# Kernel tuning notes

Measured on AMD Instinct MI355X. Metric: run time of the kernel, lower is better.

The kernel has to match this reference:

```python
import jax, jax.numpy as jnp
import numpy as np

D_MODEL = 1024
D_STATE = 64
BATCH = 4
SEQ_L = 4096
LN_EPS = 1e-5


def setup_inputs() -> dict:
    key = jax.random.key(0)
    ks = jax.random.split(key, 8)
    u = jax.random.normal(ks[0], (BATCH, SEQ_L, D_MODEL), jnp.float32)
    # Parameters mirroring StateSpaceLayer._initialize_parameters
    A_log = jax.random.uniform(ks[1], (D_STATE,), jnp.float32, -2.0, -0.1)
    xav = float(np.sqrt(6.0 / (D_STATE + D_MODEL)))
    B = jax.random.uniform(ks[2], (D_STATE, D_MODEL), jnp.float32, -xav, xav) * 0.1
    C = jax.random.uniform(ks[3], (D_MODEL, D_STATE), jnp.float32, -xav, xav) * 0.1
    D = jnp.zeros((D_MODEL,), jnp.float32)
    delta = jax.random.uniform(ks[4], (D_MODEL,), jnp.float32, 0.001, 0.1)
    gamma = jnp.ones((D_MODEL,), jnp.float32)
    beta = jnp.zeros((D_MODEL,), jnp.float32)
    freq_align = jax.random.normal(ks[5], (D_MODEL,), jnp.float32)
    reward = jax.random.normal(ks[6], (D_MODEL,), jnp.float32)
    return dict(u=u, A_log=A_log, B=B, C=C, D=D, delta=delta,
                gamma=gamma, beta=beta, freq_align=freq_align, reward=reward)


def reference(u, A_log, B, C, D, delta, gamma, beta, freq_align, reward):
    b, L, d = u.shape
    A = -jnp.exp(A_log)                                   # [N]
    # --- convolution kernel: K[k] = C @ (A_bar[0])^k, A_bar[0] = exp(delta[0]*A) ---
    k_idx = jnp.arange(L, dtype=u.dtype)                  # [L]
    powers = jnp.exp(k_idx[:, None] * (delta[0] * A)[None, :])  # [L, N]
    K = jnp.einsum('ln,dn->ld', powers, C)                # [L, D]
    # --- FFT-based causal (circular, zero-padded) convolution ---
    fft_size = 1 << int(np.ceil(np.log2(2 * L)))
    u_fft = jnp.fft.fft(u, n=fft_size, axis=1)            # [B, F, D] complex
    K_fft = jnp.fft.fft(K, n=fft_size, axis=0)            # [F, D] complex
    y = jnp.fft.ifft(u_fft * K_fft[None], axis=1).real[:, :L, :]
    # --- D skip connection ---
    y = y + u * D
    # --- FFT-based learning signals: scale spectrum, add real 'reward' to every bin ---
    y_fft = jnp.fft.fft(y, axis=1)
    y = jnp.fft.ifft(y_fft * freq_align + reward, axis=1).real
    # --- LayerNorm (eval-mode dropout = identity) ---
    mean = y.mean(-1, keepdims=True)
    var = y.var(-1, keepdims=True)
    y = (y - mean) / jnp.sqrt(var + LN_EPS) * gamma + beta
    # --- final state update with mean timescale ---
    delta_mean = delta.mean()
    A_bar_s = jnp.exp(delta_mean * A)                     # [N]
    A_safe = A + 1e-8 * jnp.sign(A)
    B_bar = ((A_bar_s - 1.0) / A_safe)[:, None] * B       # [N, D]
    state = jnp.zeros((b, A.shape[0]), u.dtype)
    final_state = A_bar_s * state + jnp.einsum('nd,bd->bn', B_bar, u[:, -1, :])
    return (y, final_state)
```

## Files before the change

### kernel.cpp

```cpp
#include <hip/hip_runtime.h>
#include <math.h>

#define BATCH  4
#define SEQL   4096
#define DMODEL 1024
#define NSTATE 64
#define LN_EPS 1e-5f
#define TB     16

typedef unsigned short u16;
typedef unsigned int   u32;
typedef float f32x2 __attribute__((ext_vector_type(2)));

__device__ __forceinline__ f32x2 fma2(f32x2 a, f32x2 b, f32x2 c) {
#if __has_builtin(__builtin_elementwise_fma)
    return __builtin_elementwise_fma(a, b, c);
#else
    f32x2 d; d.x = fmaf(a.x, b.x, c.x); d.y = fmaf(a.y, b.y, c.y); return d;
#endif
}

__device__ __forceinline__ u16 f2bf(float x) {
    u32 b = __float_as_uint(x);
    b += 0x7FFF + ((b >> 16) & 1);
    return (u16)(b >> 16);
}
__device__ __forceinline__ float bf2f(u16 h) {
    return __uint_as_float(((u32)h) << 16);
}

__global__ __launch_bounds__(256) void k_local_state(const float* __restrict__ u,
                                                     const float* __restrict__ A_log,
                                                     const float* __restrict__ delta,
                                                     const float* __restrict__ Bm,
                                                     u16* __restrict__ f,
                                                     float* __restrict__ st,
                                                     int NCH, int TCH, int nb) {
    if (blockIdx.x >= nb) {
        const int sb = blockIdx.x - nb;
        const int n = sb & 63;
        const int b = sb >> 6;
        const int tid = threadIdx.x;
        const float* ul = u + ((size_t)b * SEQL + (SEQL - 1)) * DMODEL;
        const float* Bn = Bm + (size_t)n * DMODEL;
        float dot = 0.f, dsum = 0.f;
        for (int dd = tid; dd < DMODEL; dd += 256) {
            dot = fmaf(Bn[dd], ul[dd], dot);
            dsum += delta[dd];
        }
#pragma unroll
        for (int off = 32; off > 0; off >>= 1) {
            dot  += __shfl_down(dot,  off, 64);
            dsum += __shfl_down(dsum, off, 64);
        }
        __shared__ float red[8];
        const int wave = tid >> 6, lane = tid & 63;
        if (lane == 0) { red[wave] = dot; red[4 + wave] = dsum; }
        __syncthreads();
        if (tid == 0) {
            dot  = red[0] + red[1] + red[2] + red[3];
            dsum = red[4] + red[5] + red[6] + red[7];
            const float dmean = dsum * (1.f / DMODEL);
            const float A = -expf(A_log[n]);
            const float Abar = expf(dmean * A);
            const float Asafe = A + (A >= 0.f ? 1e-8f : -1e-8f);
            st[sb] = ((Abar - 1.f) / Asafe) * dot;
        }
        return;
    }
    __shared__ float r_lds[NSTATE];
    const int tid = threadIdx.x;
    const int w = tid >> 6, l = tid & 63;
    const int b   = blockIdx.x / (16 * NCH);
    const int rem = blockIdx.x % (16 * NCH);
    const int dt  = rem / NCH;
    const int j   = rem % NCH;
    const int n0  = w << 4;
    const int d   = (dt << 6) | l;

    if (tid < NSTATE) r_lds[tid] = expf(delta[0] * -expf(A_log[tid]));
    __syncthreads();

    f32x2 r2[8], s2[8];
#pragma unroll
    for (int p = 0; p < 8; ++p) {
        r2[p] = *(const f32x2*)&r_lds[n0 + 2 * p];
        s2[p] = (f32x2)(0.f, 0.f);
    }

    const float* ub = u + ((size_t)b * SEQL + (size_t)j * TCH) * DMODEL + d;
    for (int tb = 0; tb < TCH / TB; ++tb) {
        float ur[TB];
#pragma unroll
        for (int t = 0; t < TB; ++t)
            ur[t] = ub[(size_t)(tb * TB + t) * DMODEL];
#pragma unroll
        for (int q = 0; q < 4; ++q) {
            f32x2 sa = s2[2*q], sb2 = s2[2*q+1];
            const f32x2 ra = r2[2*q], rb = r2[2*q+1];
#pragma unroll
            for (int t = 0; t < TB; ++t) {
                f32x2 u2; u2.x = ur[t]; u2.y = ur[t];
                sa  = fma2(ra, sa,  u2);
                sb2 = fma2(rb, sb2, u2);
            }
            s2[2*q] = sa; s2[2*q+1] = sb2;
        }
    }
    u16* fb = f + (((size_t)b * NCH + j) * NSTATE + n0) * DMODEL + d;
#pragma unroll
    for (int p = 0; p < 8; ++p) {
        fb[(size_t)(2*p)     * DMODEL] = f2bf(s2[p].x);
        fb[(size_t)(2*p + 1) * DMODEL] = f2bf(s2[p].y);
    }
}

template <bool ZBF16>
__global__ __launch_bounds__(256) void k_replay(const float* __restrict__ u,
                                                const float* __restrict__ A_log,
                                                const float* __restrict__ C,
                                                const float* __restrict__ Dvec,
                                                const float* __restrict__ delta,
                                                const u16* __restrict__ f,
                                                const float* __restrict__ fal,
                                                const float* __restrict__ rw,
                                                void* __restrict__ zout,
                                                int NCH, int TCH) {
    __shared__ float r_lds[NSTATE];
    __shared__ float rT_lds[NSTATE];
    __shared__ float part[2][4][TB][64];
    const int tid = threadIdx.x;
    const int w = tid >> 6, l = tid & 63;
    const int b   = blockIdx.x / (16 * NCH);
    const int rem = blockIdx.x % (16 * NCH);
    const int dt  = rem / NCH;
    const int j   = rem % NCH;
    const int n0  = w << 4;
    const int d   = (dt << 6) | l;

    if (tid < NSTATE) {
        const float A = -expf(A_log[tid]);
        const float d0v = delta[0];
        r_lds[tid]  = expf(d0v * A);
        rT_lds[tid] = expf((float)TCH * d0v * A);
    }
    __syncthreads();

    const float fad = fal[d];
    f32x2 r2[8], c2[8], s2[8];
#pragma unroll
    for (int p = 0; p < 8; ++p) {
        r2[p] = *(const f32x2*)&r_lds[n0 + 2 * p];
        s2[p] = (f32x2)(0.f, 0.f);
    }
#pragma unroll
    for (int p = 0; p < 8; ++p) {
        c2[p].x = fad * C[(size_t)d * NSTATE + n0 + 2*p];
        c2[p].y = fad * C[(size_t)d * NSTATE + n0 + 2*p + 1];
    }

    {
        f32x2 rT2[8];
#pragma unroll
        for (int p = 0; p < 8; ++p)
            rT2[p] = *(const f32x2*)&rT_lds[n0 + 2 * p];
        const u16* fbase = f + ((size_t)b * NCH * NSTATE + n0) * DMODEL + d;
        const size_t kstride = (size_t)NSTATE * DMODEL;
#pragma unroll 1
        for (int k = 0; k < j; ++k) {
            const u16* fk = fbase + (size_t)k * kstride;
#pragma unroll
            for (int p = 0; p < 8; ++p) {
                f32x2 fv;
                fv.x = bf2f(fk[(size_t)(2*p)     * DMODEL]);
                fv.y = bf2f(fk[(size_t)(2*p + 1) * DMODEL]);
                s2[p] = fma2(rT2[p], s2[p], fv);
            }
        }
    }

    const float Ddf = Dvec[d] * fad;
    const float rwd = rw[d];
    const float* ub = u + ((size_t)b * SEQL + (size_t)j * TCH) * DMODEL + d;
    const size_t zoff = ((size_t)b * SEQL + (size_t)j * TCH) * DMODEL + d;
    u16*   zb16 = (u16*)zout + zoff;
    float* zb32 = (float*)zout + zoff;

    for (int tb = 0; tb < TCH / TB; ++tb) {
        const int pb = tb & 1;
        float ur[TB];
        f32x2 zr2[TB];
#pragma unroll
        for (int t = 0; t < TB; ++t) {
            ur[t] = ub[(size_t)(tb * TB + t) * DMODEL];
            zr2[t] = (f32x2)(0.f, 0.f);
        }
#pragma unroll
        for (int q = 0; q < 4; ++q) {
            f32x2 sa = s2[2*q], sb2 = s2[2*q+1];
            const f32x2 ra = r2[2*q], rb = r2[2*q+1];
            const f32x2 ca = c2[2*q], cb = c2[2*q+1];
#pragma unroll
            for (int t = 0; t < TB; ++t) {
                f32x2 u2; u2.x = ur[t]; u2.y = ur[t];
                sa  = fma2(ra, sa,  u2);
                sb2 = fma2(rb, sb2, u2);
                zr2[t] = fma2(ca, sa,  zr2[t]);
                zr2[t] = fma2(cb, sb2, zr2[t]);
            }
            s2[2*q] = sa; s2[2*q+1] = sb2;
        }
#pragma unroll
        for (int t = 0; t < TB; ++t) {
            float v = zr2[t].x + zr2[t].y;
            if (w == 0) v = fmaf(Ddf, ur[t], v);
            part[pb][w][t][l] = v;
        }
        __syncthreads();
#pragma unroll
        for (int k = 0; k < 4; ++k) {
            const int t = (w << 2) | k;
            float v = (part[pb][0][t][l] + part[pb][1][t][l]) +
                      (part[pb][2][t][l] + part[pb][3][t][l]);
            if (j == 0 && tb == 0 && t == 0) v += rwd;
            if (ZBF16) zb16[(size_t)(tb * TB + t) * DMODEL] = f2bf(v);
            else       zb32[(size_t)(tb * TB + t) * DMODEL] = v;
        }
    }
}

template <bool ZBF16>
__global__ __launch_bounds__(256) void k_ln(const void* __restrict__ zin,
                                            float* __restrict__ y,
                                            const float* __restrict__ gamma,
                                            const float* __restrict__ beta) {
    const int tid = threadIdx.x;
    float4 v;
    if (ZBF16) {
        const ushort4 h = ((const ushort4*)((const u16*)zin + (size_t)blockIdx.x * DMODEL))[tid];
        v.x = bf2f(h.x); v.y = bf2f(h.y); v.z = bf2f(h.z); v.w = bf2f(h.w);
    } else {
        v = ((const float4*)((const float*)zin + (size_t)blockIdx.x * DMODEL))[tid];
    }
    float sum = v.x + v.y + v.z + v.w;
    float sq  = v.x*v.x + v.y*v.y + v.z*v.z + v.w*v.w;
#pragma unroll
    for (int off = 32; off > 0; off >>= 1) {
        sum += __shfl_down(sum, off, 64);
        sq  += __shfl_down(sq,  off, 64);
    }
    __shared__ float red[8];
    const int wave = tid >> 6, lane = tid & 63;
    if (lane == 0) { red[wave] = sum; red[4 + wave] = sq; }
    __syncthreads();
    sum = red[0] + red[1] + red[2] + red[3];
    sq  = red[4] + red[5] + red[6] + red[7];
    const float mean = sum * (1.f / DMODEL);
    const float var  = sq * (1.f / DMODEL) - mean * mean;
    const float inv  = 1.f / sqrtf(var + LN_EPS);
    const float4 g  = ((const float4*)gamma)[tid];
    const float4 bb = ((const float4*)beta)[tid];
    float4 o;
    o.x = (v.x - mean) * inv * g.x + bb.x;
    o.y = (v.y - mean) * inv * g.y + bb.y;
    o.z = (v.z - mean) * inv * g.z + bb.z;
    o.w = (v.w - mean) * inv * g.w + bb.w;
    ((float4*)(y + (size_t)blockIdx.x * DMODEL))[tid] = o;
}

extern "C" void kernel_launch(void* const* d_in, const int* in_sizes, int n_in,
                              void* d_out, int out_size, void* d_ws, size_t ws_size,
                              hipStream_t stream) {
    const float* u     = (const float*)d_in[0];
    const float* A_log = (const float*)d_in[1];
    const float* B     = (const float*)d_in[2];
    const float* C     = (const float*)d_in[3];
    const float* Dv    = (const float*)d_in[4];
    const float* delta = (const float*)d_in[5];
    const float* gamma = (const float*)d_in[6];
    const float* beta  = (const float*)d_in[7];
    const float* fal   = (const float*)d_in[8];
    const float* rw    = (const float*)d_in[9];

    float* y  = (float*)d_out;
    float* st = y + (size_t)BATCH * SEQL * DMODEL;
    u16* f    = (u16*)d_ws;

    int NCH = 16;
    while (NCH > 4 && (size_t)BATCH * NCH * NSTATE * DMODEL * sizeof(u16) > ws_size)
        NCH >>= 1;
    const int TCH = SEQL / NCH;
    const int nb = BATCH * 16 * NCH;

    const size_t f_bytes = (size_t)BATCH * NCH * NSTATE * DMODEL * sizeof(u16);
    const size_t z_bytes = (size_t)BATCH * SEQL * DMODEL * sizeof(u16);
    const bool zbf16 = (f_bytes + z_bytes) <= ws_size;
    void* zbuf = zbf16 ? (void*)((char*)d_ws + f_bytes) : (void*)y;

    hipLaunchKernelGGL(k_local_state, dim3(nb + BATCH * NSTATE), dim3(256), 0, stream,
                       u, A_log, delta, B, f, st, NCH, TCH, nb);
    if (zbf16) {
        hipLaunchKernelGGL((k_replay<true>), dim3(nb), dim3(256), 0, stream,
                           u, A_log, C, Dv, delta, f, fal, rw, zbuf, NCH, TCH);
        hipLaunchKernelGGL((k_ln<true>), dim3(BATCH * SEQL), dim3(256), 0, stream,
                           zbuf, y, gamma, beta);
    } else {
        hipLaunchKernelGGL((k_replay<false>), dim3(nb), dim3(256), 0, stream,
                           u, A_log, C, Dv, delta, f, fal, rw, zbuf, NCH, TCH);
        hipLaunchKernelGGL((k_ln<false>), dim3(BATCH * SEQL), dim3(256), 0, stream,
                           zbuf, y, gamma, beta);
    }
}
```

Before: 120.2 us.

## Restructure chunked scan: local scan first, carry pass, then fused correction+LayerNorm

Replaces the local-state pass plus replay pass with a single chunk-local scan that writes the partial output z and each chunk's end state. A small kernel then scans the chunk carries across chunks and stores C-weighted carries. A fused kernel adds the carry's decayed contribution to z and applies LayerNorm, with eight rows per block. This removes the second full read of u and the per-chunk O(j) carry replay, at the cost of a 64-state correction GEMV per row in the LayerNorm kernel and an extra launch. NCH is now fixed at 16 instead of adapting to workspace size.

```diff
diff --git a/kernel.cpp b/kernel.cpp
--- a/kernel.cpp
+++ b/kernel.cpp
@@ -6,7 +6,10 @@
 #define DMODEL 1024
 #define NSTATE 64
 #define LN_EPS 1e-5f
+#define NCH    16
+#define TCH    256
 #define TB     16
+#define TSUB   8
 
 typedef unsigned short u16;
 typedef unsigned int   u32;
@@ -28,14 +31,23 @@
 __device__ __forceinline__ float bf2f(u16 h) {
     return __uint_as_float(((u32)h) << 16);
 }
-
-__global__ __launch_bounds__(256) void k_local_state(const float* __restrict__ u,
-                                                     const float* __restrict__ A_log,
-                                                     const float* __restrict__ delta,
-                                                     const float* __restrict__ Bm,
-                                                     u16* __restrict__ f,
-                                                     float* __restrict__ st,
-                                                     int NCH, int TCH, int nb) {
+__device__ __forceinline__ f32x2 unpack2bf(u32 p) {
+    f32x2 v; v.x = bf2f((u16)p); v.y = bf2f((u16)(p >> 16)); return v;
+}
+
+template <bool ZBF16>
+__global__ __launch_bounds__(256) void k_scan(const float* __restrict__ u,
+                                              const float* __restrict__ A_log,
+                                              const float* __restrict__ C,
+                                              const float* __restrict__ Dvec,
+                                              const float* __restrict__ delta,
+                                              const float* __restrict__ fal,
+                                              const float* __restrict__ rw,
+                                              const float* __restrict__ Bm,
+                                              u16* __restrict__ f,
+                                              void* __restrict__ zout,
+                                              float* __restrict__ st,
+                                              int nb) {
     if (blockIdx.x >= nb) {
         const int sb = blockIdx.x - nb;
         const int n = sb & 63;
@@ -69,65 +81,6 @@
         return;
     }
     __shared__ float r_lds[NSTATE];
-    const int tid = threadIdx.x;
-    const int w = tid >> 6, l = tid & 63;
-    const int b   = blockIdx.x / (16 * NCH);
-    const int rem = blockIdx.x % (16 * NCH);
-    const int dt  = rem / NCH;
-    const int j   = rem % NCH;
-    const int n0  = w << 4;
-    const int d   = (dt << 6) | l;
-
-    if (tid < NSTATE) r_lds[tid] = expf(delta[0] * -expf(A_log[tid]));
-    __syncthreads();
-
-    f32x2 r2[8], s2[8];
-#pragma unroll
-    for (int p = 0; p < 8; ++p) {
-        r2[p] = *(const f32x2*)&r_lds[n0 + 2 * p];
-        s2[p] = (f32x2)(0.f, 0.f);
-    }
-
-    const float* ub = u + ((size_t)b * SEQL + (size_t)j * TCH) * DMODEL + d;
-    for (int tb = 0; tb < TCH / TB; ++tb) {
-        float ur[TB];
-#pragma unroll
-        for (int t = 0; t < TB; ++t)
-            ur[t] = ub[(size_t)(tb * TB + t) * DMODEL];
-#pragma unroll
-        for (int q = 0; q < 4; ++q) {
-            f32x2 sa = s2[2*q], sb2 = s2[2*q+1];
-            const f32x2 ra = r2[2*q], rb = r2[2*q+1];
-#pragma unroll
-            for (int t = 0; t < TB; ++t) {
-                f32x2 u2; u2.x = ur[t]; u2.y = ur[t];
-                sa  = fma2(ra, sa,  u2);
-                sb2 = fma2(rb, sb2, u2);
-            }
-            s2[2*q] = sa; s2[2*q+1] = sb2;
-        }
-    }
-    u16* fb = f + (((size_t)b * NCH + j) * NSTATE + n0) * DMODEL + d;
-#pragma unroll
-    for (int p = 0; p < 8; ++p) {
-        fb[(size_t)(2*p)     * DMODEL] = f2bf(s2[p].x);
-        fb[(size_t)(2*p + 1) * DMODEL] = f2bf(s2[p].y);
-    }
-}
-
-template <bool ZBF16>
-__global__ __launch_bounds__(256) void k_replay(const float* __restrict__ u,
-                                                const float* __restrict__ A_log,
-                                                const float* __restrict__ C,
-                                                const float* __restrict__ Dvec,
-                                                const float* __restrict__ delta,
-                                                const u16* __restrict__ f,
-                                                const float* __restrict__ fal,
-                                                const float* __restrict__ rw,
-                                                void* __restrict__ zout,
-                                                int NCH, int TCH) {
-    __shared__ float r_lds[NSTATE];
-    __shared__ float rT_lds[NSTATE];
     __shared__ float part[2][4][TB][64];
     const int tid = threadIdx.x;
     const int w = tid >> 6, l = tid & 63;
@@ -138,12 +91,7 @@
     const int n0  = w << 4;
     const int d   = (dt << 6) | l;
 
-    if (tid < NSTATE) {
-        const float A = -expf(A_log[tid]);
-        const float d0v = delta[0];
-        r_lds[tid]  = expf(d0v * A);
-        rT_lds[tid] = expf((float)TCH * d0v * A);
-    }
+    if (tid < NSTATE) r_lds[tid] = expf(delta[0] * -expf(A_log[tid]));
     __syncthreads();
 
     const float fad = fal[d];
@@ -157,26 +105,6 @@
     for (int p = 0; p < 8; ++p) {
         c2[p].x = fad * C[(size_t)d * NSTATE + n0 + 2*p];
         c2[p].y = fad * C[(size_t)d * NSTATE + n0 + 2*p + 1];
-    }
-
-    {
-        f32x2 rT2[8];
-#pragma unroll
-        for (int p = 0; p < 8; ++p)
-            rT2[p] = *(const f32x2*)&rT_lds[n0 + 2 * p];
-        const u16* fbase = f + ((size_t)b * NCH * NSTATE + n0) * DMODEL + d;
-        const size_t kstride = (size_t)NSTATE * DMODEL;
-#pragma unroll 1
-        for (int k = 0; k < j; ++k) {
-            const u16* fk = fbase + (size_t)k * kstride;
-#pragma unroll
-            for (int p = 0; p < 8; ++p) {
-                f32x2 fv;
-                fv.x = bf2f(fk[(size_t)(2*p)     * DMODEL]);
-                fv.y = bf2f(fk[(size_t)(2*p + 1) * DMODEL]);
-                s2[p] = fma2(rT2[p], s2[p], fv);
-            }
-        }
     }
 
     const float Ddf = Dvec[d] * fad;
@@ -227,45 +155,142 @@
             else       zb32[(size_t)(tb * TB + t) * DMODEL] = v;
         }
     }
+    u16* fb = f + (((size_t)b * NCH + j) * NSTATE + n0) * DMODEL + d;
+#pragma unroll
+    for (int p = 0; p < 8; ++p) {
+        fb[(size_t)(2*p)     * DMODEL] = f2bf(s2[p].x);
+        fb[(size_t)(2*p + 1) * DMODEL] = f2bf(s2[p].y);
+    }
+}
+
+__global__ __launch_bounds__(256) void k_pass2w(const float* __restrict__ A_log,
+                                                const float* __restrict__ delta,
+                                                const float* __restrict__ C,
+                                                const float* __restrict__ fal,
+                                                u16* __restrict__ f) {
+    const int tid = blockIdx.x * 256 + threadIdx.x;
+    const int d = tid & (DMODEL - 1);
+    const int n = (tid >> 10) & (NSTATE - 1);
+    const int b = tid >> 16;
+    const float A  = -expf(A_log[n]);
+    const float rT = expf((float)TCH * delta[0] * A);
+    const float fc = fal[d] * C[(size_t)d * NSTATE + n];
+    float I = 0.f;
+    u16* p = f + ((size_t)b * NCH * NSTATE + n) * DMODEL + d;
+    const size_t stride = (size_t)NSTATE * DMODEL;
+    for (int j = 0; j < NCH; ++j) {
+        float tmp = bf2f(p[(size_t)j * stride]);
+        p[(size_t)j * stride] = f2bf(fc * I);
+        I = fmaf(rT, I, tmp);
+    }
 }
 
 template <bool ZBF16>
-__global__ __launch_bounds__(256) void k_ln(const void* __restrict__ zin,
-                                            float* __restrict__ y,
-                                            const float* __restrict__ gamma,
-                                            const float* __restrict__ beta) {
+__global__ __launch_bounds__(256) void k_corr_ln(const void* __restrict__ zin,
+                                                 const u16* __restrict__ W,
+                                                 const float* __restrict__ A_log,
+                                                 const float* __restrict__ delta,
+                                                 const float* __restrict__ gamma,
+                                                 const float* __restrict__ beta,
+                                                 float* __restrict__ y) {
+    const int lb  = (blockIdx.x & 7) * 256 + (blockIdx.x >> 3);
+    const int b   = lb >> 9;
+    const int row = lb & 511;
+    const int tbase = row * TSUB;
+    const int j     = tbase >> 8;
+    const int tloc0 = tbase & (TCH - 1);
+
+    __shared__ float r_lds[NSTATE];
+    __shared__ float pst_lds[NSTATE];
+    __shared__ float red[4 * TSUB * 2];
+
     const int tid = threadIdx.x;
-    float4 v;
-    if (ZBF16) {
-        const ushort4 h = ((const ushort4*)((const u16*)zin + (size_t)blockIdx.x * DMODEL))[tid];
-        v.x = bf2f(h.x); v.y = bf2f(h.y); v.z = bf2f(h.z); v.w = bf2f(h.w);
-    } else {
-        v = ((const float4*)((const float*)zin + (size_t)blockIdx.x * DMODEL))[tid];
-    }
-    float sum = v.x + v.y + v.z + v.w;
-    float sq  = v.x*v.x + v.y*v.y + v.z*v.z + v.w*v.w;
-#pragma unroll
-    for (int off = 32; off > 0; off >>= 1) {
-        sum += __shfl_down(sum, off, 64);
-        sq  += __shfl_down(sq,  off, 64);
-    }
-    __shared__ float red[8];
+    if (tid < NSTATE) {
+        const float A = -expf(A_log[tid]);
+        const float d0v = delta[0];
+        r_lds[tid]   = expf(d0v * A);
+        pst_lds[tid] = expf((float)(tloc0 + 1) * d0v * A);
+    }
+    __syncthreads();
+
+    const int d0 = tid << 2;
+    f32x2 acc01[TSUB], acc23[TSUB];
+#pragma unroll
+    for (int t = 0; t < TSUB; ++t) {
+        acc01[t] = (f32x2)(0.f, 0.f);
+        acc23[t] = (f32x2)(0.f, 0.f);
+    }
+
+    if (j > 0) {
+        const u16* Wb = W + (((size_t)b * NCH + j) * NSTATE) * DMODEL + d0;
+#pragma unroll 2
+        for (int n = 0; n < NSTATE; ++n) {
+            const uint2 wv = *(const uint2*)(Wb + (size_t)n * DMODEL);
+            const f32x2 w01 = unpack2bf(wv.x);
+            const f32x2 w23 = unpack2bf(wv.y);
+            float p = pst_lds[n];
+            const float r = r_lds[n];
+#pragma unroll
+            for (int t = 0; t < TSUB; ++t) {
+                f32x2 pp; pp.x = p; pp.y = p;
+                acc01[t] = fma2(pp, w01, acc01[t]);
+                acc23[t] = fma2(pp, w23, acc23[t]);
+                p *= r;
+            }
+        }
+    }
+
+    const size_t rowoff = ((size_t)b * SEQL + tbase) * DMODEL + d0;
+    float sums[TSUB], sqs[TSUB];
+#pragma unroll
+    for (int t = 0; t < TSUB; ++t) {
+        float z0, z1, z2, z3;
+        if (ZBF16) {
+            const uint2 zv = *(const uint2*)((const u16*)zin + rowoff + (size_t)t * DMODEL);
+            const f32x2 a = unpack2bf(zv.x), bb2 = unpack2bf(zv.y);
+            z0 = a.x; z1 = a.y; z2 = bb2.x; z3 = bb2.y;
+        } else {
+            const float4 zv = *(const float4*)((const float*)zin + rowoff + (size_t)t * DMODEL);
+            z0 = zv.x; z1 = zv.y; z2 = zv.z; z3 = zv.w;
+        }
+        z0 += acc01[t].x; z1 += acc01[t].y; z2 += acc23[t].x; z3 += acc23[t].y;
+        acc01[t].x = z0; acc01[t].y = z1; acc23[t].x = z2; acc23[t].y = z3;
+        sums[t] = (z0 + z1) + (z2 + z3);
+        sqs[t]  = (z0*z0 + z1*z1) + (z2*z2 + z3*z3);
+    }
     const int wave = tid >> 6, lane = tid & 63;
-    if (lane == 0) { red[wave] = sum; red[4 + wave] = sq; }
+#pragma unroll
+    for (int t = 0; t < TSUB; ++t) {
+        float s = sums[t], q = sqs[t];
+#pragma unroll
+        for (int off = 32; off > 0; off >>= 1) {
+            s += __shfl_down(s, off, 64);
+            q += __shfl_down(q, off, 64);
+        }
+        if (lane == 0) {
+            red[(wave * TSUB + t) * 2]     = s;
+            red[(wave * TSUB + t) * 2 + 1] = q;
+        }
+    }
     __syncthreads();
-    sum = red[0] + red[1] + red[2] + red[3];
-    sq  = red[4] + red[5] + red[6] + red[7];
-    const float mean = sum * (1.f / DMODEL);
-    const float var  = sq * (1.f / DMODEL) - mean * mean;
-    const float inv  = 1.f / sqrtf(var + LN_EPS);
-    const float4 g  = ((const float4*)gamma)[tid];
-    const float4 bb = ((const float4*)beta)[tid];
-    float4 o;
-    o.x = (v.x - mean) * inv * g.x + bb.x;
-    o.y = (v.y - mean) * inv * g.y + bb.y;
-    o.z = (v.z - mean) * inv * g.z + bb.z;
-    o.w = (v.w - mean) * inv * g.w + bb.w;
-    ((float4*)(y + (size_t)blockIdx.x * DMODEL))[tid] = o;
+    const float4 g  = *(const float4*)&gamma[d0];
+    const float4 bb = *(const float4*)&beta[d0];
+#pragma unroll
+    for (int t = 0; t < TSUB; ++t) {
+        float s = red[t * 2]     + red[(TSUB + t) * 2] +
+                  red[(2 * TSUB + t) * 2] + red[(3 * TSUB + t) * 2];
+        float q = red[t * 2 + 1] + red[(TSUB + t) * 2 + 1] +
+                  red[(2 * TSUB + t) * 2 + 1] + red[(3 * TSUB + t) * 2 + 1];
+        const float mean = s * (1.f / DMODEL);
+        const float var  = q * (1.f / DMODEL) - mean * mean;
+        const float inv  = 1.f / sqrtf(var + LN_EPS);
+        float4 o;
+        o.x = (acc01[t].x - mean) * inv * g.x + bb.x;
+        o.y = (acc01[t].y - mean) * inv * g.y + bb.y;
+        o.z = (acc23[t].x - mean) * inv * g.z + bb.z;
+        o.w = (acc23[t].y - mean) * inv * g.w + bb.w;
+        *(float4*)&y[rowoff + (size_t)t * DMODEL] = o;
+    }
 }
 
 extern "C" void kernel_launch(void* const* d_in, const int* in_sizes, int n_in,
@@ -286,10 +311,6 @@
     float* st = y + (size_t)BATCH * SEQL * DMODEL;
     u16* f    = (u16*)d_ws;
 
-    int NCH = 16;
-    while (NCH > 4 && (size_t)BATCH * NCH * NSTATE * DMODEL * sizeof(u16) > ws_size)
-        NCH >>= 1;
-    const int TCH = SEQL / NCH;
     const int nb = BATCH * 16 * NCH;
 
     const size_t f_bytes = (size_t)BATCH * NCH * NSTATE * DMODEL * sizeof(u16);
@@ -297,17 +318,20 @@
     const bool zbf16 = (f_bytes + z_bytes) <= ws_size;
     void* zbuf = zbf16 ? (void*)((char*)d_ws + f_bytes) : (void*)y;
 
-    hipLaunchKernelGGL(k_local_state, dim3(nb + BATCH * NSTATE), dim3(256), 0, stream,
-                       u, A_log, delta, B, f, st, NCH, TCH, nb);
     if (zbf16) {
-        hipLaunchKernelGGL((k_replay<true>), dim3(nb), dim3(256), 0, stream,
-                           u, A_log, C, Dv, delta, f, fal, rw, zbuf, NCH, TCH);
-        hipLaunchKernelGGL((k_ln<true>), dim3(BATCH * SEQL), dim3(256), 0, stream,
-                           zbuf, y, gamma, beta);
+        hipLaunchKernelGGL((k_scan<true>), dim3(nb + BATCH * NSTATE), dim3(256), 0, stream,
+                           u, A_log, C, Dv, delta, fal, rw, B, f, zbuf, st, nb);
     } else {
-        hipLaunchKernelGGL((k_replay<false>), dim3(nb), dim3(256), 0, stream,
-                           u, A_log, C, Dv, delta, f, fal, rw, zbuf, NCH, TCH);
-        hipLaunchKernelGGL((k_ln<false>), dim3(BATCH * SEQL), dim3(256), 0, stream,
-                           zbuf, y, gamma, beta);
-    }
-}
+        hipLaunchKernelGGL((k_scan<false>), dim3(nb + BATCH * NSTATE), dim3(256), 0, stream,
+                           u, A_log, C, Dv, delta, fal, rw, B, f, zbuf, st, nb);
+    }
+    hipLaunchKernelGGL(k_pass2w, dim3(BATCH * NSTATE * DMODEL / 256), dim3(256), 0, stream,
+                       A_log, delta, C, fal, f);
+    if (zbf16) {
+        hipLaunchKernelGGL((k_corr_ln<true>), dim3(BATCH * (SEQL / TSUB)), dim3(256), 0, stream,
+                           zbuf, f, A_log, delta, gamma, beta, y);
+    } else {
+        hipLaunchKernelGGL((k_corr_ln<false>), dim3(BATCH * (SEQL / TSUB)), dim3(256), 0, stream,
+                           zbuf, f, A_log, delta, gamma, beta, y);
+    }
+}
```

Result: faster. 115.2 us, median of 4 (-4.2%).
